# Performance work log

Hardware: AMD Instinct MI355X
Metric: run time of the kernel (lower is better)

Reference implementation:

```python
import jax, jax.numpy as jnp
import numpy as np

N_NODES = 50000      # nodes per side (12500 tetrahedra x 4 nodes)
N_GRAPHS = 12500     # graph pairs in the batch
HID = 256


def _tet_edges(n_graphs):
    # 12 directed edges among the 4 nodes of each tetrahedron
    pat = np.array([(a, b) for a in range(4) for b in range(4) if a != b], dtype=np.int64)  # [12,2]
    base = np.arange(n_graphs, dtype=np.int64)[:, None, None] * 4  # [G,1,1]
    ei = (base + pat[None]).reshape(-1, 2).T  # [2, 12*G]
    return jnp.asarray(ei)


def setup_inputs() -> dict:
    key = jax.random.key(0)
    ks = jax.random.split(key, 20)

    def w(k, shape, fan_in):
        return (jax.random.normal(k, shape, dtype=jnp.float32) / np.sqrt(fan_in)).astype(jnp.float32)

    x_1 = jax.random.normal(ks[0], (N_NODES, 3), dtype=jnp.float32)
    x_2 = jax.random.normal(ks[1], (N_NODES, 3), dtype=jnp.float32)
    edge_index_1 = _tet_edges(N_GRAPHS)
    edge_index_2 = _tet_edges(N_GRAPHS)
    batch_1 = jnp.repeat(jnp.arange(N_GRAPHS, dtype=jnp.int64), 4)
    batch_2 = batch_1

    params = dict(
        W1=w(ks[2], (3, HID), 3), b1=jnp.zeros((HID,), jnp.float32),
        W2=w(ks[3], (HID, HID), HID), b2=jnp.zeros((HID,), jnp.float32),
        W3=w(ks[4], (HID, HID), HID), b3=jnp.zeros((HID,), jnp.float32),
        Wl1=w(ks[5], (512, 512), 512), bl1=jnp.zeros((512,), jnp.float32),
        Wl2=w(ks[6], (512, 256), 512), bl2=jnp.zeros((256,), jnp.float32),
        Wl3=w(ks[7], (256, 128), 256), bl3=jnp.zeros((128,), jnp.float32),
        Wl4=w(ks[8], (128, 64), 128), bl4=jnp.zeros((64,), jnp.float32),
    )
    return dict(x_1=x_1, edge_index_1=edge_index_1, batch_1=batch_1,
                x_2=x_2, edge_index_2=edge_index_2, batch_2=batch_2, **params)


def gcn_conv(x, edge_index, W, b):
    # PyG GCNConv: add self loops, symmetric deg normalization, sum aggregate, then bias
    n = x.shape[0]
    loops = jnp.arange(n, dtype=edge_index.dtype)
    src = jnp.concatenate([edge_index[0], loops])
    dst = jnp.concatenate([edge_index[1], loops])
    deg = jax.ops.segment_sum(jnp.ones_like(dst, dtype=x.dtype), dst, num_segments=n)
    dis = jnp.where(deg > 0, jax.lax.rsqrt(jnp.maximum(deg, 1.0)), 0.0)
    norm = dis[src] * dis[dst]                       # [E+N]
    xw = x @ W                                       # [N, out]
    out = jax.ops.segment_sum(norm[:, None] * xw[src], dst, num_segments=n)
    return out + b


def encode(x, edge_index, batch, W1, b1, W2, b2, W3, b3):
    x = jax.nn.relu(gcn_conv(x, edge_index, W1, b1))
    x = jax.nn.relu(gcn_conv(x, edge_index, W2, b2))
    x = jax.nn.relu(gcn_conv(x, edge_index, W3, b3))
    # global_mean_pool
    s = jax.ops.segment_sum(x, batch, num_segments=N_GRAPHS)
    cnt = jax.ops.segment_sum(jnp.ones((x.shape[0],), x.dtype), batch, num_segments=N_GRAPHS)
    return s / jnp.maximum(cnt, 1.0)[:, None]


def reference(x_1, edge_index_1, batch_1, x_2, edge_index_2, batch_2,
              W1, b1, W2, b2, W3, b3,
              Wl1, bl1, Wl2, bl2, Wl3, bl3, Wl4, bl4):
    h1 = encode(x_1, edge_index_1, batch_1, W1, b1, W2, b2, W3, b3)
    h2 = encode(x_2, edge_index_2, batch_2, W1, b1, W2, b2, W3, b3)
    h = jnp.concatenate([h1, h2], axis=1)            # [G, 512]
    h = jax.nn.relu(h @ Wl1 + bl1)
    h = jax.nn.relu(h @ Wl2 + bl2)
    h = jax.nn.relu(h @ Wl3 + bl3)
    h = h @ Wl4 + bl4                                # layer_4: no relu (as in source)
    return jax.nn.sigmoid(h)                         # [G, 64]
```

## Files before the change

### kernel.cpp

```cpp
#include <hip/hip_runtime.h>


typedef _Float16 half8 __attribute__((ext_vector_type(8)));
typedef float floatx4 __attribute__((ext_vector_type(4)));

struct PrepArgsV10 { const float* in[6]; };

__global__ __launch_bounds__(256) void v10_prep(PrepArgsV10 p, _Float16* Bf) {
  const int sz[6]  = {65536, 65536, 262144, 131072, 32768, 8192};
  const int lgN[6] = {8, 8, 9, 8, 7, 6};
  const int off[6] = {0, 65536, 131072, 393216, 524288, 557056};
  int e = blockIdx.x * 256 + threadIdx.x;
  for (int i = 0; i < 6; ++i) {
    if (e < sz[i]) {
      int N = 1 << lgN[i];
      int k = e >> lgN[i];
      int n = e & (N - 1);
      float w = p.in[i][e];
      int kb = k >> 5, quad = (k >> 3) & 3, j = k & 7;
      int nt = n >> 4, l16 = n & 15;
      int lane = quad * 16 + l16;
      int dst = ((kb * (N >> 4) + nt) * 64 + lane) * 8 + j;
      Bf[off[i] + dst] = (_Float16)w;
      return;
    }
    e -= sz[i];
  }
}

template<int MT, int NT, int KB, bool ENC_IN, int OUT_MODE>
__device__ __forceinline__ void layer(
    const _Float16* __restrict__ Bf, const float* __restrict__ bias,
    _Float16* sA, float* __restrict__ outg, int pair0, int wave, int lane) {
  const int quad = lane >> 4, lr = lane & 15;
  const int n0 = wave * (NT * 16);
  const _Float16* bp = Bf + ((size_t)(wave * NT) * 64 + lane) * 8;

  floatx4 acc[MT][NT];
#pragma unroll
  for (int mt = 0; mt < MT; ++mt)
#pragma unroll
    for (int nt = 0; nt < NT; ++nt)
      acc[mt][nt] = (floatx4){0.f, 0.f, 0.f, 0.f};

  half8 bbuf[2][NT];
#pragma unroll
  for (int nt = 0; nt < NT; ++nt)
    bbuf[0][nt] = *(const half8*)(bp + nt * 512);

#pragma unroll 2
  for (int kb = 0; kb < KB; ++kb) {
    const int cur = kb & 1, nxt = cur ^ 1;
    if (kb + 1 < KB) {
#pragma unroll
      for (int nt = 0; nt < NT; ++nt)
        bbuf[nxt][nt] = *(const half8*)(bp + (size_t)(kb + 1) * (NT * 2048) + nt * 512);
    }
    half8 av[MT];
#pragma unroll
    for (int mt = 0; mt < MT; ++mt) {
      int addr = (mt * 16 + lr) * (ENC_IN ? 264 : 520) + kb * 32 + quad * 8;
      av[mt] = *(const half8*)(sA + addr);
    }
#pragma unroll
    for (int nt = 0; nt < NT; ++nt)
#pragma unroll
      for (int mt = 0; mt < MT; ++mt)
        acc[mt][nt] = __builtin_amdgcn_mfma_f32_16x16x32_f16(av[mt], bbuf[cur][nt], acc[mt][nt], 0, 0, 0);
  }

  __syncthreads();

#pragma unroll
  for (int nt = 0; nt < NT; ++nt) {
    int c = n0 + nt * 16 + lr;
    float bv = bias[c];
#pragma unroll
    for (int mt = 0; mt < MT; ++mt) {
#pragma unroll
      for (int reg = 0; reg < 4; ++reg) {
        int r = mt * 16 + quad * 4 + reg;
        float v = acc[mt][nt][reg] + bv;
        if (OUT_MODE <= 2) {
          v = fmaxf(v, 0.f);
          int a;
          if (OUT_MODE == 0)      a = r * 264 + c;
          else if (OUT_MODE == 1) a = (r >> 1) * 520 + (r & 1) * 256 + c;
          else                    a = r * 520 + c;
          sA[a] = (_Float16)v;
        } else {
          int p = pair0 + r;
          if (p < 12500) outg[(size_t)p * 64 + c] = 1.0f / (1.0f + expf(-v));
        }
      }
    }
  }
  __syncthreads();
}

__global__ __launch_bounds__(256) void v10_mega(
    const float* __restrict__ x1, const float* __restrict__ x2,
    const float* __restrict__ W1, const float* __restrict__ b1,
    const _Float16* __restrict__ Bf,
    const float* __restrict__ b2, const float* __restrict__ b3,
    const float* __restrict__ bl1, const float* __restrict__ bl2,
    const float* __restrict__ bl3, const float* __restrict__ bl4,
    float* __restrict__ outg) {
  __shared__ _Float16 sA[16896];
  __shared__ float sM[64][3];

  int tid = threadIdx.x;
  int wave = tid >> 6, lane = tid & 63;
  int pair0 = blockIdx.x * 32;

  if (tid < 64) {
    int r = tid;
    int g = pair0 + (r >> 1);
    const float* xp = (r & 1) ? x2 : x1;
    float a0 = 0.f, a1 = 0.f, a2 = 0.f;
    if (g < 12500) {
      const float* q = xp + (size_t)g * 12;
      a0 = 0.25f * (q[0] + q[3] + q[6] + q[9]);
      a1 = 0.25f * (q[1] + q[4] + q[7] + q[10]);
      a2 = 0.25f * (q[2] + q[5] + q[8] + q[11]);
    }
    sM[r][0] = a0; sM[r][1] = a1; sM[r][2] = a2;
  }
  __syncthreads();

  {
    int c = tid;
    float w0 = W1[c], w1 = W1[256 + c], w2 = W1[512 + c], bb = b1[c];
#pragma unroll 4
    for (int r = 0; r < 64; ++r) {
      float v = fmaxf(sM[r][0] * w0 + sM[r][1] * w1 + sM[r][2] * w2 + bb, 0.f);
      sA[r * 264 + c] = (_Float16)v;
    }
  }
  __syncthreads();

  layer<4, 4, 8, true, 0>(Bf + 0,      b2,  sA, nullptr, pair0, wave, lane);
  layer<4, 4, 8, true, 1>(Bf + 65536,  b3,  sA, nullptr, pair0, wave, lane);
  layer<2, 8, 16, false, 2>(Bf + 131072, bl1, sA, nullptr, pair0, wave, lane);
  layer<2, 4, 16, false, 2>(Bf + 393216, bl2, sA, nullptr, pair0, wave, lane);
  layer<2, 2, 8, false, 2>(Bf + 524288, bl3, sA, nullptr, pair0, wave, lane);
  layer<2, 1, 4, false, 3>(Bf + 557056, bl4, sA, outg,    pair0, wave, lane);
}

extern "C" void kernel_launch(void* const* d_in, const int* in_sizes, int n_in,
                              void* d_out, int out_size, void* d_ws, size_t ws_size,
                              hipStream_t stream) {
  const float* x1  = (const float*)d_in[0];
  const float* x2  = (const float*)d_in[3];
  const float* W1  = (const float*)d_in[6];
  const float* b1  = (const float*)d_in[7];
  const float* W2  = (const float*)d_in[8];
  const float* b2  = (const float*)d_in[9];
  const float* W3  = (const float*)d_in[10];
  const float* b3  = (const float*)d_in[11];
  const float* Wl1 = (const float*)d_in[12];
  const float* bl1 = (const float*)d_in[13];
  const float* Wl2 = (const float*)d_in[14];
  const float* bl2 = (const float*)d_in[15];
  const float* Wl3 = (const float*)d_in[16];
  const float* bl3 = (const float*)d_in[17];
  const float* Wl4 = (const float*)d_in[18];
  const float* bl4 = (const float*)d_in[19];

  _Float16* Bf = (_Float16*)d_ws;

  PrepArgsV10 pa;
  pa.in[0] = W2;  pa.in[1] = W3;  pa.in[2] = Wl1;
  pa.in[3] = Wl2; pa.in[4] = Wl3; pa.in[5] = Wl4;

  v10_prep<<<dim3(2208), dim3(256), 0, stream>>>(pa, Bf);
  v10_mega<<<dim3(391), dim3(256), 0, stream>>>(x1, x2, W1, b1, Bf,
                                                b2, b3, bl1, bl2, bl3, bl4,
                                                (float*)d_out);
}
```

Before: 128.7 us.

## Switch hidden layers to 32x32x16 MFMA with matching weight layout

Replaces the 16x16x32 MFMA tiles with 32x32x16 MFMA for the first five layers, which means repacking the fp16 weights in the prep kernel and changing the A-fragment and accumulator indexing. Larger MFMA tiles are meant to reduce the number of LDS A-loads and B-fragment loads per FLOP and improve matrix-core utilization. The final sigmoid layer keeps the 16x16 path because its width is only 64. It also adds an occupancy hint to the launch bounds, which may force register spills given the larger 16-wide accumulators.

```diff
diff --git a/kernel.cpp b/kernel.cpp
--- a/kernel.cpp
+++ b/kernel.cpp
@@ -3,10 +3,11 @@
 
 typedef _Float16 half8 __attribute__((ext_vector_type(8)));
 typedef float floatx4 __attribute__((ext_vector_type(4)));
-
-struct PrepArgsV10 { const float* in[6]; };
-
-__global__ __launch_bounds__(256) void v10_prep(PrepArgsV10 p, _Float16* Bf) {
+typedef float floatx16 __attribute__((ext_vector_type(16)));
+
+struct PrepArgsV11 { const float* in[6]; };
+
+__global__ __launch_bounds__(256) void v11_prep(PrepArgsV11 p, _Float16* Bf) {
   const int sz[6]  = {65536, 65536, 262144, 131072, 32768, 8192};
   const int lgN[6] = {8, 8, 9, 8, 7, 6};
   const int off[6] = {0, 65536, 131072, 393216, 524288, 557056};
@@ -17,10 +18,18 @@
       int k = e >> lgN[i];
       int n = e & (N - 1);
       float w = p.in[i][e];
-      int kb = k >> 5, quad = (k >> 3) & 3, j = k & 7;
-      int nt = n >> 4, l16 = n & 15;
-      int lane = quad * 16 + l16;
-      int dst = ((kb * (N >> 4) + nt) * 64 + lane) * 8 + j;
+      int dst;
+      if (i < 5) {
+        int kb = k >> 4, half = (k >> 3) & 1, j = k & 7;
+        int nt = n >> 5;
+        int lane = half * 32 + (n & 31);
+        dst = ((kb * (N >> 5) + nt) * 64 + lane) * 8 + j;
+      } else {
+        int kb = k >> 5, quad = (k >> 3) & 3, j = k & 7;
+        int nt = n >> 4;
+        int lane = quad * 16 + (n & 15);
+        dst = ((kb * (N >> 4) + nt) * 64 + lane) * 8 + j;
+      }
       Bf[off[i] + dst] = (_Float16)w;
       return;
     }
@@ -29,7 +38,71 @@
 }
 
 template<int MT, int NT, int KB, bool ENC_IN, int OUT_MODE>
-__device__ __forceinline__ void layer(
+__device__ __forceinline__ void layer32(
+    const _Float16* __restrict__ Bf, const float* __restrict__ bias,
+    _Float16* sA, int wave, int lane) {
+  const int n5 = lane & 31, khalf = lane >> 5;
+  const int n0 = wave * (NT * 32);
+  const int STRIDE = ENC_IN ? 264 : 520;
+  const _Float16* bp = Bf + ((size_t)(wave * NT) * 64 + lane) * 8;
+
+  floatx16 acc[MT][NT];
+#pragma unroll
+  for (int mt = 0; mt < MT; ++mt)
+#pragma unroll
+    for (int nt = 0; nt < NT; ++nt)
+#pragma unroll
+      for (int q = 0; q < 16; ++q) acc[mt][nt][q] = 0.f;
+
+  half8 bbuf[2][NT];
+#pragma unroll
+  for (int nt = 0; nt < NT; ++nt)
+    bbuf[0][nt] = *(const half8*)(bp + nt * 512);
+
+#pragma unroll 2
+  for (int kb = 0; kb < KB; ++kb) {
+    const int cur = kb & 1, nxt = cur ^ 1;
+    if (kb + 1 < KB) {
+#pragma unroll
+      for (int nt = 0; nt < NT; ++nt)
+        bbuf[nxt][nt] = *(const half8*)(bp + (size_t)(kb + 1) * (NT * 2048) + nt * 512);
+    }
+    half8 av[MT];
+#pragma unroll
+    for (int mt = 0; mt < MT; ++mt)
+      av[mt] = *(const half8*)(sA + (mt * 32 + n5) * STRIDE + kb * 16 + khalf * 8);
+#pragma unroll
+    for (int nt = 0; nt < NT; ++nt)
+#pragma unroll
+      for (int mt = 0; mt < MT; ++mt)
+        acc[mt][nt] = __builtin_amdgcn_mfma_f32_32x32x16_f16(av[mt], bbuf[cur][nt], acc[mt][nt], 0, 0, 0);
+  }
+
+  __syncthreads();
+
+#pragma unroll
+  for (int nt = 0; nt < NT; ++nt) {
+    int c = n0 + nt * 32 + n5;
+    float bv = bias[c];
+#pragma unroll
+    for (int mt = 0; mt < MT; ++mt) {
+#pragma unroll
+      for (int reg = 0; reg < 16; ++reg) {
+        int r = mt * 32 + (reg & 3) + 8 * (reg >> 2) + 4 * khalf;
+        float v = fmaxf(acc[mt][nt][reg] + bv, 0.f);
+        int a;
+        if (OUT_MODE == 0)      a = r * 264 + c;
+        else if (OUT_MODE == 1) a = (r >> 1) * 520 + (r & 1) * 256 + c;
+        else                    a = r * 520 + c;
+        sA[a] = (_Float16)v;
+      }
+    }
+  }
+  __syncthreads();
+}
+
+template<int MT, int NT, int KB>
+__device__ __forceinline__ void layer16_out(
     const _Float16* __restrict__ Bf, const float* __restrict__ bias,
     _Float16* sA, float* __restrict__ outg, int pair0, int wave, int lane) {
   const int quad = lane >> 4, lr = lane & 15;
@@ -58,17 +131,14 @@
     }
     half8 av[MT];
 #pragma unroll
-    for (int mt = 0; mt < MT; ++mt) {
-      int addr = (mt * 16 + lr) * (ENC_IN ? 264 : 520) + kb * 32 + quad * 8;
-      av[mt] = *(const half8*)(sA + addr);
-    }
+    for (int mt = 0; mt < MT; ++mt)
+      av[mt] = *(const half8*)(sA + (mt * 16 + lr) * 520 + kb * 32 + quad * 8);
 #pragma unroll
     for (int nt = 0; nt < NT; ++nt)
 #pragma unroll
       for (int mt = 0; mt < MT; ++mt)
         acc[mt][nt] = __builtin_amdgcn_mfma_f32_16x16x32_f16(av[mt], bbuf[cur][nt], acc[mt][nt], 0, 0, 0);
   }
-
   __syncthreads();
 
 #pragma unroll
@@ -81,24 +151,15 @@
       for (int reg = 0; reg < 4; ++reg) {
         int r = mt * 16 + quad * 4 + reg;
         float v = acc[mt][nt][reg] + bv;
-        if (OUT_MODE <= 2) {
-          v = fmaxf(v, 0.f);
-          int a;
-          if (OUT_MODE == 0)      a = r * 264 + c;
-          else if (OUT_MODE == 1) a = (r >> 1) * 520 + (r & 1) * 256 + c;
-          else                    a = r * 520 + c;
-          sA[a] = (_Float16)v;
-        } else {
-          int p = pair0 + r;
-          if (p < 12500) outg[(size_t)p * 64 + c] = 1.0f / (1.0f + expf(-v));
-        }
+        int p = pair0 + r;
+        if (p < 12500) outg[(size_t)p * 64 + c] = 1.0f / (1.0f + expf(-v));
       }
     }
   }
   __syncthreads();
 }
 
-__global__ __launch_bounds__(256) void v10_mega(
+__global__ __launch_bounds__(256, 3) void v11_mega(
     const float* __restrict__ x1, const float* __restrict__ x2,
     const float* __restrict__ W1, const float* __restrict__ b1,
     const _Float16* __restrict__ Bf,
@@ -139,12 +200,12 @@
   }
   __syncthreads();
 
-  layer<4, 4, 8, true, 0>(Bf + 0,      b2,  sA, nullptr, pair0, wave, lane);
-  layer<4, 4, 8, true, 1>(Bf + 65536,  b3,  sA, nullptr, pair0, wave, lane);
-  layer<2, 8, 16, false, 2>(Bf + 131072, bl1, sA, nullptr, pair0, wave, lane);
-  layer<2, 4, 16, false, 2>(Bf + 393216, bl2, sA, nullptr, pair0, wave, lane);
-  layer<2, 2, 8, false, 2>(Bf + 524288, bl3, sA, nullptr, pair0, wave, lane);
-  layer<2, 1, 4, false, 3>(Bf + 557056, bl4, sA, outg,    pair0, wave, lane);
+  layer32<2, 2, 16, true, 0>(Bf + 0,      b2,  sA, wave, lane);
+  layer32<2, 2, 16, true, 1>(Bf + 65536,  b3,  sA, wave, lane);
+  layer32<1, 4, 32, false, 2>(Bf + 131072, bl1, sA, wave, lane);
+  layer32<1, 2, 32, false, 2>(Bf + 393216, bl2, sA, wave, lane);
+  layer32<1, 1, 16, false, 2>(Bf + 524288, bl3, sA, wave, lane);
+  layer16_out<2, 1, 4>(Bf + 557056, bl4, sA, outg, pair0, wave, lane);
 }
 
 extern "C" void kernel_launch(void* const* d_in, const int* in_sizes, int n_in,
@@ -169,12 +230,12 @@
 
   _Float16* Bf = (_Float16*)d_ws;
 
-  PrepArgsV10 pa;
+  PrepArgsV11 pa;
   pa.in[0] = W2;  pa.in[1] = W3;  pa.in[2] = Wl1;
   pa.in[3] = Wl2; pa.in[4] = Wl3; pa.in[5] = Wl4;
 
-  v10_prep<<<dim3(2208), dim3(256), 0, stream>>>(pa, Bf);
-  v10_mega<<<dim3(391), dim3(256), 0, stream>>>(x1, x2, W1, b1, Bf,
+  v11_prep<<<dim3(2208), dim3(256), 0, stream>>>(pa, Bf);
+  v11_mega<<<dim3(391), dim3(256), 0, stream>>>(x1, x2, W1, b1, Bf,
                                                 b2, b3, bl1, bl2, bl3, bl4,
                                                 (float*)d_out);
 }
```

After: 130.1 us. Within noise of the previous version (+1.1%).

## Use 50-pair 512-thread blocks with 8 waves and triple-buffered weight prefetch

Applied to the files above, without the earlier changes.

Each block now handles 50 graph pairs (112 padded rows) with 8 waves instead of 32 pairs with 4 waves, so the grid drops from 391 to 250 blocks. That is roughly one block per CU, and each weight tile loaded from global memory is reused over more rows. The B-fragment prefetch becomes a fully unrolled triple buffer issued two k-steps ahead. Padded rows are zero-filled, and the last layer splits waves across M. In exchange, LDS use doubles, register pressure rises from MT=7 accumulators, and padding adds wasted MFMA work on 12 of 112 rows.

```diff
diff --git a/kernel.cpp b/kernel.cpp
--- a/kernel.cpp
+++ b/kernel.cpp
@@ -4,9 +4,9 @@
 typedef _Float16 half8 __attribute__((ext_vector_type(8)));
 typedef float floatx4 __attribute__((ext_vector_type(4)));
 
-struct PrepArgsV10 { const float* in[6]; };
+struct PrepArgsV12 { const float* in[6]; };
 
-__global__ __launch_bounds__(256) void v10_prep(PrepArgsV10 p, _Float16* Bf) {
+__global__ __launch_bounds__(256) void v12_prep(PrepArgsV12 p, _Float16* Bf) {
   const int sz[6]  = {65536, 65536, 262144, 131072, 32768, 8192};
   const int lgN[6] = {8, 8, 9, 8, 7, 6};
   const int off[6] = {0, 65536, 131072, 393216, 524288, 557056};
@@ -18,8 +18,8 @@
       int n = e & (N - 1);
       float w = p.in[i][e];
       int kb = k >> 5, quad = (k >> 3) & 3, j = k & 7;
-      int nt = n >> 4, l16 = n & 15;
-      int lane = quad * 16 + l16;
+      int nt = n >> 4;
+      int lane = quad * 16 + (n & 15);
       int dst = ((kb * (N >> 4) + nt) * 64 + lane) * 8 + j;
       Bf[off[i] + dst] = (_Float16)w;
       return;
@@ -28,13 +28,14 @@
   }
 }
 
-template<int MT, int NT, int KB, bool ENC_IN, int OUT_MODE>
+template<int MT, int NT, int TNT, int KB, bool ENC_IN, int OUT_MODE>
 __device__ __forceinline__ void layer(
     const _Float16* __restrict__ Bf, const float* __restrict__ bias,
-    _Float16* sA, float* __restrict__ outg, int pair0, int wave, int lane) {
+    _Float16* sA, float* __restrict__ outg, int pair0, int nw, int m0, int lane) {
   const int quad = lane >> 4, lr = lane & 15;
-  const int n0 = wave * (NT * 16);
-  const _Float16* bp = Bf + ((size_t)(wave * NT) * 64 + lane) * 8;
+  const int n0 = nw * (NT * 16);
+  const int STRIDE = ENC_IN ? 264 : 520;
+  const _Float16* bp = Bf + ((size_t)(nw * NT) * 64 + lane) * 8;
 
   floatx4 acc[MT][NT];
 #pragma unroll
@@ -43,30 +44,31 @@
     for (int nt = 0; nt < NT; ++nt)
       acc[mt][nt] = (floatx4){0.f, 0.f, 0.f, 0.f};
 
-  half8 bbuf[2][NT];
+  half8 bbuf[3][NT];
 #pragma unroll
-  for (int nt = 0; nt < NT; ++nt)
+  for (int nt = 0; nt < NT; ++nt) {
     bbuf[0][nt] = *(const half8*)(bp + nt * 512);
+    bbuf[1][nt] = *(const half8*)(bp + (size_t)TNT * 512 + nt * 512);
+  }
 
-#pragma unroll 2
+#pragma unroll
   for (int kb = 0; kb < KB; ++kb) {
-    const int cur = kb & 1, nxt = cur ^ 1;
-    if (kb + 1 < KB) {
-#pragma unroll
-      for (int nt = 0; nt < NT; ++nt)
-        bbuf[nxt][nt] = *(const half8*)(bp + (size_t)(kb + 1) * (NT * 2048) + nt * 512);
-    }
+    const int cur = kb % 3;
     half8 av[MT];
 #pragma unroll
-    for (int mt = 0; mt < MT; ++mt) {
-      int addr = (mt * 16 + lr) * (ENC_IN ? 264 : 520) + kb * 32 + quad * 8;
-      av[mt] = *(const half8*)(sA + addr);
-    }
+    for (int mt = 0; mt < MT; ++mt)
+      av[mt] = *(const half8*)(sA + (m0 + mt * 16 + lr) * STRIDE + kb * 32 + quad * 8);
 #pragma unroll
     for (int nt = 0; nt < NT; ++nt)
 #pragma unroll
       for (int mt = 0; mt < MT; ++mt)
         acc[mt][nt] = __builtin_amdgcn_mfma_f32_16x16x32_f16(av[mt], bbuf[cur][nt], acc[mt][nt], 0, 0, 0);
+    if (kb + 2 < KB) {
+      const int nxt = (kb + 2) % 3;
+#pragma unroll
+      for (int nt = 0; nt < NT; ++nt)
+        bbuf[nxt][nt] = *(const half8*)(bp + (size_t)(kb + 2) * (TNT * 512) + nt * 512);
+    }
   }
 
   __syncthreads();
@@ -79,7 +81,7 @@
     for (int mt = 0; mt < MT; ++mt) {
 #pragma unroll
       for (int reg = 0; reg < 4; ++reg) {
-        int r = mt * 16 + quad * 4 + reg;
+        int r = m0 + mt * 16 + quad * 4 + reg;
         float v = acc[mt][nt][reg] + bv;
         if (OUT_MODE <= 2) {
           v = fmaxf(v, 0.f);
@@ -89,8 +91,7 @@
           else                    a = r * 520 + c;
           sA[a] = (_Float16)v;
         } else {
-          int p = pair0 + r;
-          if (p < 12500) outg[(size_t)p * 64 + c] = 1.0f / (1.0f + expf(-v));
+          if (r < 50) outg[(size_t)(pair0 + r) * 64 + c] = 1.0f / (1.0f + expf(-v));
         }
       }
     }
@@ -98,7 +99,7 @@
   __syncthreads();
 }
 
-__global__ __launch_bounds__(256) void v10_mega(
+__global__ __launch_bounds__(512, 2) void v12_mega(
     const float* __restrict__ x1, const float* __restrict__ x2,
     const float* __restrict__ W1, const float* __restrict__ b1,
     const _Float16* __restrict__ Bf,
@@ -106,20 +107,21 @@
     const float* __restrict__ bl1, const float* __restrict__ bl2,
     const float* __restrict__ bl3, const float* __restrict__ bl4,
     float* __restrict__ outg) {
-  __shared__ _Float16 sA[16896];
-  __shared__ float sM[64][3];
+  __shared__ _Float16 sA[33280];
+  __shared__ float sM[112][3];
 
   int tid = threadIdx.x;
   int wave = tid >> 6, lane = tid & 63;
-  int pair0 = blockIdx.x * 32;
+  int pair0 = blockIdx.x * 50;
 
-  if (tid < 64) {
+  for (int i = tid; i < 16640; i += 512) ((float*)sA)[i] = 0.f;
+
+  if (tid < 112) {
     int r = tid;
-    int g = pair0 + (r >> 1);
-    const float* xp = (r & 1) ? x2 : x1;
     float a0 = 0.f, a1 = 0.f, a2 = 0.f;
-    if (g < 12500) {
-      const float* q = xp + (size_t)g * 12;
+    if (r < 100) {
+      int g = pair0 + (r >> 1);
+      const float* q = ((r & 1) ? x2 : x1) + (size_t)g * 12;
       a0 = 0.25f * (q[0] + q[3] + q[6] + q[9]);
       a1 = 0.25f * (q[1] + q[4] + q[7] + q[10]);
       a2 = 0.25f * (q[2] + q[5] + q[8] + q[11]);
@@ -129,22 +131,22 @@
   __syncthreads();
 
   {
-    int c = tid;
+    int c = tid & 255;
     float w0 = W1[c], w1 = W1[256 + c], w2 = W1[512 + c], bb = b1[c];
-#pragma unroll 4
-    for (int r = 0; r < 64; ++r) {
+    for (int r = (tid >> 8); r < 112; r += 2) {
       float v = fmaxf(sM[r][0] * w0 + sM[r][1] * w1 + sM[r][2] * w2 + bb, 0.f);
       sA[r * 264 + c] = (_Float16)v;
     }
   }
   __syncthreads();
 
-  layer<4, 4, 8, true, 0>(Bf + 0,      b2,  sA, nullptr, pair0, wave, lane);
-  layer<4, 4, 8, true, 1>(Bf + 65536,  b3,  sA, nullptr, pair0, wave, lane);
-  layer<2, 8, 16, false, 2>(Bf + 131072, bl1, sA, nullptr, pair0, wave, lane);
-  layer<2, 4, 16, false, 2>(Bf + 393216, bl2, sA, nullptr, pair0, wave, lane);
-  layer<2, 2, 8, false, 2>(Bf + 524288, bl3, sA, nullptr, pair0, wave, lane);
-  layer<2, 1, 4, false, 3>(Bf + 557056, bl4, sA, outg,    pair0, wave, lane);
+  layer<7, 2, 16,  8, true,  0>(Bf + 0,      b2,  sA, nullptr, pair0, wave, 0, lane);
+  layer<7, 2, 16,  8, true,  1>(Bf + 65536,  b3,  sA, nullptr, pair0, wave, 0, lane);
+  layer<4, 4, 32, 16, false, 2>(Bf + 131072, bl1, sA, nullptr, pair0, wave, 0, lane);
+  layer<4, 2, 16, 16, false, 2>(Bf + 393216, bl2, sA, nullptr, pair0, wave, 0, lane);
+  layer<4, 1,  8,  8, false, 2>(Bf + 524288, bl3, sA, nullptr, pair0, wave, 0, lane);
+  layer<2, 1,  4,  4, false, 3>(Bf + 557056, bl4, sA, outg,    pair0,
+                                wave & 3, (wave >> 2) * 32, lane);
 }
 
 extern "C" void kernel_launch(void* const* d_in, const int* in_sizes, int n_in,
@@ -169,12 +171,12 @@
 
   _Float16* Bf = (_Float16*)d_ws;
 
-  PrepArgsV10 pa;
+  PrepArgsV12 pa;
   pa.in[0] = W2;  pa.in[1] = W3;  pa.in[2] = Wl1;
   pa.in[3] = Wl2; pa.in[4] = Wl3; pa.in[5] = Wl4;
 
-  v10_prep<<<dim3(2208), dim3(256), 0, stream>>>(pa, Bf);
-  v10_mega<<<dim3(391), dim3(256), 0, stream>>>(x1, x2, W1, b1, Bf,
+  v12_prep<<<dim3(2208), dim3(256), 0, stream>>>(pa, Bf);
+  v12_mega<<<dim3(250), dim3(512), 0, stream>>>(x1, x2, W1, b1, Bf,
                                                 b2, b3, bl1, bl2, bl3, bl4,
                                                 (float*)d_out);
 }
```

Result: faster. 122.3 us (-5.0%).
